# Kernel optimization log

Measured on AMD Instinct MI355X. Metric: run time of the kernel, lower is better.

Reference implementation:

```python
import math
import jax, jax.numpy as jnp
import numpy as np

HEADS = 2
HEAD_NUMS = 4
BS, C, NR, NC = 16, 256, 96, 96


def _sa(x, mask, kw, kb, qw, qb, vw, vb):
    # x: [B, C, N] (Conv1d k=1 == per-position linear), mask: [B, N] floats in {0,1}
    B, Cc, N = x.shape
    H = HEAD_NUMS
    D = Cc // H
    scale = 1.0 / math.sqrt(D)

    def proj(w, b):
        return (jnp.einsum('dc,bcn->bdn', w, x) + b[None, :, None]).reshape(B, H, D, N)

    k = proj(kw, kb)
    q = proj(qw, qb)
    v = proj(vw, vb)
    # logits[b,h,n,m] = sum_d k[b,h,d,n] * q[b,h,d,m]; softmax over m, mask on m
    logits = jnp.einsum('bhdn,bhdm->bhnm', k, q) * scale
    mbool = mask > 0
    logits = jnp.where(mbool[:, None, None, :], logits, jnp.asarray(-1e30, x.dtype))
    w = jax.nn.softmax(logits, axis=-1)
    out = jnp.einsum('bhdm,bhnm->bhdn', v, w).reshape(B, Cc, N)
    # fully-masked sequences (padded grid rows/cols) -> zero instead of NaN
    valid = jnp.any(mbool, axis=-1)  # [B]
    out = jnp.where(valid[:, None, None], out, jnp.zeros((), x.dtype))
    return out + x


def setup_inputs() -> dict:
    key = jax.random.key(0)
    ks = jax.random.split(key, 16)
    num_rows = jax.random.randint(ks[0], (BS,), NR // 2, NR + 1, dtype=jnp.int32)
    num_cols = jax.random.randint(ks[1], (BS,), NC // 2, NC + 1, dtype=jnp.int32)
    feats = jax.random.normal(ks[2], (BS, C, NR, NC), dtype=jnp.float32)
    # aligned cell features are zero in padded region (align_cells_feat pads with 0)
    rmask = (jnp.arange(NR)[None, :] < num_rows[:, None])
    cmask = (jnp.arange(NC)[None, :] < num_cols[:, None])
    grid = (rmask[:, :, None] & cmask[:, None, :]).astype(jnp.float32)
    feats = feats * grid[:, None, :, :]
    inp = {'feats': feats, 'num_rows': num_rows, 'num_cols': num_cols}
    names = ['col_k', 'col_q', 'col_v', 'row_k', 'row_q', 'row_v']
    for i, nm in enumerate(names):
        inp[nm + '_w'] = 0.02 * jax.random.normal(ks[3 + 2 * i], (HEADS, C, C), dtype=jnp.float32)
        inp[nm + '_b'] = 0.02 * jax.random.normal(ks[4 + 2 * i], (HEADS, C), dtype=jnp.float32)
    return inp


def reference(feats, num_rows, num_cols,
              col_k_w, col_k_b, col_q_w, col_q_b, col_v_w, col_v_b,
              row_k_w, row_k_b, row_q_w, row_q_b, row_v_w, row_v_b):
    bs, c, nr, nc = feats.shape
    rmask = (jnp.arange(nr)[None, :] < num_rows[:, None])
    cmask = (jnp.arange(nc)[None, :] < num_cols[:, None])
    masks = (rmask[:, :, None] & cmask[:, None, :]).astype(feats.dtype)  # [bs, nr, nc]
    x = feats
    for i in range(HEADS):
        # column attention: sequences along nc, one per (batch, row)
        xc = x.transpose(0, 2, 1, 3).reshape(bs * nr, c, nc)
        mc = masks.reshape(bs * nr, nc)
        xc = _sa(xc, mc, col_k_w[i], col_k_b[i], col_q_w[i], col_q_b[i], col_v_w[i], col_v_b[i])
        x = xc.reshape(bs, nr, c, nc).transpose(0, 2, 1, 3)
        # row attention: sequences along nr, one per (batch, col)
        xr = x.transpose(0, 3, 1, 2).reshape(bs * nc, c, nr)
        mr = masks.transpose(0, 2, 1).reshape(bs * nc, nr)
        xr = _sa(xr, mr, row_k_w[i], row_k_b[i], row_q_w[i], row_q_b[i], row_v_w[i], row_v_b[i])
        x = xr.reshape(bs, nc, c, nr).transpose(0, 2, 3, 1)
    return x, masks
```

## Files before the change

### kernel.cpp

```cpp
#include <hip/hip_runtime.h>

typedef __attribute__((ext_vector_type(8))) short bf16x8;
typedef __attribute__((ext_vector_type(4))) float f32x4;

#define MFMA16(a, b, c) __builtin_amdgcn_mfma_f32_16x16x32_bf16(a, b, c, 0, 0, 0)

__device__ __forceinline__ unsigned short f2bf(float f) {
    unsigned int u = __float_as_uint(f);
    u += 0x7FFFu + ((u >> 16) & 1u);
    return (unsigned short)(u >> 16);
}
__device__ __forceinline__ float bf2f(unsigned short h) {
    return __uint_as_float(((unsigned int)h) << 16);
}

struct WPtrs { const float* p[6]; };

__global__ __launch_bounds__(256) void conv_w_kernel(WPtrs wp, unsigned short* dst) {
    int idx = blockIdx.x * 256 + threadIdx.x;
    if (idx >= 196608) return;
    int t = idx >> 15;
    int q = idx & 32767;
    float4 v = *(const float4*)(wp.p[t] + ((size_t)q << 2));
    ushort4 o;
    o.x = f2bf(v.x); o.y = f2bf(v.y); o.z = f2bf(v.z); o.w = f2bf(v.w);
    *(ushort4*)(dst + ((size_t)t << 17) + ((size_t)q << 2)) = o;
}

__global__ __launch_bounds__(256) void conv_in_kernel(const float* __restrict__ src,
                                                      unsigned short* __restrict__ dst, int n4) {
    for (int i = blockIdx.x * 256 + threadIdx.x; i < n4; i += gridDim.x * 256) {
        float4 v = *(const float4*)(src + 4 * (size_t)i);
        ushort4 o;
        o.x = f2bf(v.x); o.y = f2bf(v.y); o.z = f2bf(v.z); o.w = f2bf(v.w);
        *(ushort4*)(dst + 4 * (size_t)i) = o;
    }
}

__global__ __launch_bounds__(256) void transpose_ip(unsigned short* __restrict__ x) {
    __shared__ unsigned short t[96 * 98];
    const size_t base = (size_t)blockIdx.x * 9216;
    for (int i = threadIdx.x; i < 2304; i += 256) {
        int r = i / 24, c4 = (i % 24) * 4;
        ushort4 v = *(const ushort4*)(x + base + r * 96 + c4);
        t[r * 98 + c4 + 0] = v.x; t[r * 98 + c4 + 1] = v.y;
        t[r * 98 + c4 + 2] = v.z; t[r * 98 + c4 + 3] = v.w;
    }
    __syncthreads();
    for (int i = threadIdx.x; i < 2304; i += 256) {
        int r = i / 24, c4 = (i % 24) * 4;
        ushort4 o;
        o.x = t[(c4 + 0) * 98 + r]; o.y = t[(c4 + 1) * 98 + r];
        o.z = t[(c4 + 2) * 98 + r]; o.w = t[(c4 + 3) * 98 + r];
        *(ushort4*)(x + base + r * 96 + c4) = o;
    }
}

__global__ __launch_bounds__(256) void final_t(const unsigned short* __restrict__ x,
                                               float* __restrict__ out) {
    __shared__ unsigned short t[96 * 98];
    const size_t base = (size_t)blockIdx.x * 9216;
    for (int i = threadIdx.x; i < 2304; i += 256) {
        int r = i / 24, c4 = (i % 24) * 4;
        ushort4 v = *(const ushort4*)(x + base + r * 96 + c4);
        t[r * 98 + c4 + 0] = v.x; t[r * 98 + c4 + 1] = v.y;
        t[r * 98 + c4 + 2] = v.z; t[r * 98 + c4 + 3] = v.w;
    }
    __syncthreads();
    for (int i = threadIdx.x; i < 2304; i += 256) {
        int r = i / 24, c4 = (i % 24) * 4;
        float4 f;
        f.x = bf2f(t[(c4 + 0) * 98 + r]); f.y = bf2f(t[(c4 + 1) * 98 + r]);
        f.z = bf2f(t[(c4 + 2) * 98 + r]); f.w = bf2f(t[(c4 + 3) * 98 + r]);
        *(float4*)(out + base + r * 96 + c4) = f;
    }
}

__global__ __launch_bounds__(256) void masks_kernel(const int* __restrict__ nr,
                                                    const int* __restrict__ nc,
                                                    float* __restrict__ out) {
    int i = blockIdx.x * 256 + threadIdx.x;
    if (i >= 147456) return;
    int b = i / 9216, rem = i % 9216, r = rem / 96, c = rem % 96;
    out[i] = (r < nr[b] && c < nc[b]) ? 1.0f : 0.0f;
}

#define XT_S 40
#define KT_S 72
#define VM_S 104
#define PM_S 104
#define OT_S 100

__global__ __launch_bounds__(384, 3) void sa2(
    const unsigned short* __restrict__ src, unsigned short* __restrict__ dst,
    const unsigned short* __restrict__ Wk, const unsigned short* __restrict__ Wq,
    const unsigned short* __restrict__ Wv,
    const float* __restrict__ bk, const float* __restrict__ bq, const float* __restrict__ bv,
    const int* __restrict__ lim_s, const int* __restrict__ lim_m) {
    extern __shared__ char smem[];
    unsigned short* xt = (unsigned short*)smem;
    unsigned short* Kt = (unsigned short*)(smem + 7680);
    unsigned short* Qt = (unsigned short*)(smem + 21504);
    unsigned short* Vm = (unsigned short*)(smem + 35328);
    unsigned short* Pm = (unsigned short*)(smem + 48640);
    float*          OT = (float*)smem;

    const int bid = blockIdx.x;
    const int h   = bid & 3;
    const int seq = bid >> 2;
    const int b = seq / 96, s = seq % 96;
    const int tid = threadIdx.x;

    const size_t slab = (size_t)b * 2359296 + (size_t)s * 96;
    const unsigned short* sg = src + slab;
    unsigned short* dg = dst + slab;

    if (s >= lim_s[b]) {
        for (int i = tid; i < 768; i += 384) {
            int c = h * 64 + i / 12, o8 = (i % 12) * 8;
            *(uint4*)(dg + (size_t)c * 9216 + o8) = *(const uint4*)(sg + (size_t)c * 9216 + o8);
        }
        return;
    }
    const int mlim = lim_m[b];

    const int wave = tid >> 6, lane = tid & 63, lr = lane & 15, lk = lane >> 4;
    const int p = wave >> 1, g = wave & 1;
    const unsigned short* Wp = (p == 0) ? Wk : (p == 1) ? Wq : Wv;
    const float* bp = (p == 0) ? bk : (p == 1) ? bq : bv;

    const int cloc = tid / 12, oc = tid % 12;
    f32x4 acc[2][6];
#pragma unroll
    for (int dt = 0; dt < 2; ++dt)
#pragma unroll
        for (int nt = 0; nt < 6; ++nt) acc[dt][nt] = (f32x4)0.0f;

    uint4 v = *(const uint4*)(sg + (size_t)cloc * 9216 + oc * 8);
#pragma unroll
    for (int cc = 0; cc < 8; ++cc) {
        __syncthreads();
        {
            const unsigned short* pv = (const unsigned short*)&v;
#pragma unroll
            for (int j = 0; j < 8; ++j) {
                const int jj = (j + cloc) & 7;
                xt[(oc * 8 + jj) * XT_S + cloc] = pv[jj];
            }
        }
        __syncthreads();
        if (cc < 7) v = *(const uint4*)(sg + (size_t)((cc + 1) * 32 + cloc) * 9216 + oc * 8);
        bf16x8 bfr[6];
#pragma unroll
        for (int nt = 0; nt < 6; ++nt)
            bfr[nt] = *(const bf16x8*)&xt[(nt * 16 + lr) * XT_S + lk * 8];
#pragma unroll
        for (int dt = 0; dt < 2; ++dt) {
            bf16x8 afr = *(const bf16x8*)&Wp[(size_t)(h * 64 + g * 32 + dt * 16 + lr) * 256 + cc * 32 + lk * 8];
#pragma unroll
            for (int nt = 0; nt < 6; ++nt)
                acc[dt][nt] = MFMA16(afr, bfr[nt], acc[dt][nt]);
        }
    }

#pragma unroll
    for (int dt = 0; dt < 2; ++dt) {
        const int dbase = g * 32 + dt * 16 + lk * 4;
        const float b0 = bp[h * 64 + dbase + 0], b1 = bp[h * 64 + dbase + 1];
        const float b2 = bp[h * 64 + dbase + 2], b3 = bp[h * 64 + dbase + 3];
#pragma unroll
        for (int nt = 0; nt < 6; ++nt) {
            const int n = nt * 16 + lr;
            if (p == 2) {
                Vm[(dbase + 0) * VM_S + n] = f2bf(acc[dt][nt][0] + b0);
                Vm[(dbase + 1) * VM_S + n] = f2bf(acc[dt][nt][1] + b1);
                Vm[(dbase + 2) * VM_S + n] = f2bf(acc[dt][nt][2] + b2);
                Vm[(dbase + 3) * VM_S + n] = f2bf(acc[dt][nt][3] + b3);
            } else {
                ushort4 o;
                o.x = f2bf(acc[dt][nt][0] + b0);
                o.y = f2bf(acc[dt][nt][1] + b1);
                o.z = f2bf(acc[dt][nt][2] + b2);
                o.w = f2bf(acc[dt][nt][3] + b3);
                *(ushort4*)&((p == 0 ? Kt : Qt)[n * KT_S + dbase]) = o;
            }
        }
    }
    __syncthreads();

    f32x4 acc2[6];
#pragma unroll
    for (int mt = 0; mt < 6; ++mt) acc2[mt] = (f32x4)0.0f;
#pragma unroll
    for (int k0 = 0; k0 < 64; k0 += 32) {
        bf16x8 kf = *(const bf16x8*)&Kt[(wave * 16 + lr) * KT_S + k0 + lk * 8];
#pragma unroll
        for (int mt = 0; mt < 6; ++mt) {
            bf16x8 qf = *(const bf16x8*)&Qt[(mt * 16 + lr) * KT_S + k0 + lk * 8];
            acc2[mt] = MFMA16(kf, qf, acc2[mt]);
        }
    }

    float lg[6][4];
#pragma unroll
    for (int mt = 0; mt < 6; ++mt) {
        const bool valid = (mt * 16 + lr) < mlim;
#pragma unroll
        for (int r2 = 0; r2 < 4; ++r2)
            lg[mt][r2] = valid ? acc2[mt][r2] * 0.125f : -3.0e38f;
    }
#pragma unroll
    for (int r2 = 0; r2 < 4; ++r2) {
        float mx = lg[0][r2];
#pragma unroll
        for (int mt = 1; mt < 6; ++mt) mx = fmaxf(mx, lg[mt][r2]);
        mx = fmaxf(mx, __shfl_xor(mx, 1));
        mx = fmaxf(mx, __shfl_xor(mx, 2));
        mx = fmaxf(mx, __shfl_xor(mx, 4));
        mx = fmaxf(mx, __shfl_xor(mx, 8));
        float sm = 0.0f;
#pragma unroll
        for (int mt = 0; mt < 6; ++mt) {
            float e = __expf(lg[mt][r2] - mx);
            lg[mt][r2] = e;
            sm += e;
        }
        sm += __shfl_xor(sm, 1);
        sm += __shfl_xor(sm, 2);
        sm += __shfl_xor(sm, 4);
        sm += __shfl_xor(sm, 8);
        const float inv = 1.0f / sm;
        const int n = wave * 16 + lk * 4 + r2;
#pragma unroll
        for (int mt = 0; mt < 6; ++mt)
            Pm[n * PM_S + mt * 16 + lr] = f2bf(lg[mt][r2] * inv);
    }
    __syncthreads();

    f32x4 acc3[4];
#pragma unroll
    for (int dt = 0; dt < 4; ++dt) acc3[dt] = (f32x4)0.0f;
    const int nk = (mlim + 31) >> 5;
    for (int k0i = 0; k0i < nk; ++k0i) {
        const int k0 = k0i * 32;
        bf16x8 pf = *(const bf16x8*)&Pm[(wave * 16 + lr) * PM_S + k0 + lk * 8];
#pragma unroll
        for (int dt = 0; dt < 4; ++dt) {
            bf16x8 vf = *(const bf16x8*)&Vm[(dt * 16 + lr) * VM_S + k0 + lk * 8];
            acc3[dt] = MFMA16(vf, pf, acc3[dt]);
        }
    }

#pragma unroll
    for (int dt = 0; dt < 4; ++dt)
#pragma unroll
        for (int r2 = 0; r2 < 4; ++r2)
            OT[(dt * 16 + lk * 4 + r2) * OT_S + wave * 16 + lr] = acc3[dt][r2];
    __syncthreads();
    for (int i = tid; i < 768; i += 384) {
        const int c = i / 12, o8 = (i % 12) * 8;
        const size_t ga = (size_t)(h * 64 + c) * 9216 + o8;
        uint4 rv = *(const uint4*)(sg + ga);
        const unsigned short* rs = (const unsigned short*)&rv;
        unsigned short ob[8];
#pragma unroll
        for (int j = 0; j < 8; ++j)
            ob[j] = f2bf(OT[c * OT_S + o8 + j] + bf2f(rs[j]));
        *(uint4*)(dg + ga) = *(const uint4*)ob;
    }
}

extern "C" void kernel_launch(void* const* d_in, const int* in_sizes, int n_in,
                              void* d_out, int out_size, void* d_ws, size_t ws_size,
                              hipStream_t stream) {
    const float* feats    = (const float*)d_in[0];
    const int*   num_rows = (const int*)d_in[1];
    const int*   num_cols = (const int*)d_in[2];

    unsigned short* bufA = (unsigned short*)d_ws;
    unsigned short* wbuf = (unsigned short*)((char*)d_ws + 75497472);
    unsigned short* bufB = (unsigned short*)d_out;

    WPtrs wp;
    for (int t = 0; t < 6; ++t) wp.p[t] = (const float*)d_in[3 + 2 * t];

    (void)hipFuncSetAttribute((const void*)sa2,
                              hipFuncAttributeMaxDynamicSharedMemorySize, 68608);

    conv_w_kernel<<<768, 256, 0, stream>>>(wp, wbuf);
    conv_in_kernel<<<2048, 256, 0, stream>>>(feats, bufA, 9437184);

    unsigned short* cur = bufA;
    unsigned short* nxt = bufB;
    for (int i = 0; i < 2; ++i) {
        for (int dir = 0; dir < 2; ++dir) {
            const int tb = dir * 3;
            const unsigned short* Wk = wbuf + (size_t)(tb + 0) * 131072 + (size_t)i * 65536;
            const unsigned short* Wq = wbuf + (size_t)(tb + 1) * 131072 + (size_t)i * 65536;
            const unsigned short* Wv = wbuf + (size_t)(tb + 2) * 131072 + (size_t)i * 65536;
            const float* bk = (const float*)d_in[4 + 2 * (tb + 0)] + i * 256;
            const float* bq = (const float*)d_in[4 + 2 * (tb + 1)] + i * 256;
            const float* bv = (const float*)d_in[4 + 2 * (tb + 2)] + i * 256;
            const int* lim_s = (dir == 0) ? num_rows : num_cols;
            const int* lim_m = (dir == 0) ? num_cols : num_rows;
            sa2<<<6144, 384, 68608, stream>>>(cur, nxt, Wk, Wq, Wv, bk, bq, bv, lim_s, lim_m);
            unsigned short* t = cur; cur = nxt; nxt = t;
            if (!(i == 1 && dir == 1))
                transpose_ip<<<4096, 256, 0, stream>>>(cur);
        }
    }

    final_t<<<4096, 256, 0, stream>>>(cur, (float*)d_out);
    masks_kernel<<<576, 256, 0, stream>>>(num_rows, num_cols, (float*)d_out + 37748736);
}
```

Baseline: 1.328 ms.

## Switch to channel-last layout with transposing writes, dropping separate transpose passes

The activation layout becomes channel-innermost ([b, r, c, C]). The attention kernel now reads B fragments straight from global memory without the LDS staging transpose, and writes its output already transposed for the next direction, so the three transpose_ip launches go away. The input conversion and final output kernels now also transpose. Shared memory is reused across phases (Pm/OT alias Kt), which cuts it to 40KB and lifts occupancy to 4 blocks, at the cost of extra barriers. Blocks are also reordered so neighbouring sequences share weight and cache locality.

```diff
diff --git a/kernel.cpp b/kernel.cpp
--- a/kernel.cpp
+++ b/kernel.cpp
@@ -27,52 +27,51 @@
     *(ushort4*)(dst + ((size_t)t << 17) + ((size_t)q << 2)) = o;
 }
 
-__global__ __launch_bounds__(256) void conv_in_kernel(const float* __restrict__ src,
-                                                      unsigned short* __restrict__ dst, int n4) {
-    for (int i = blockIdx.x * 256 + threadIdx.x; i < n4; i += gridDim.x * 256) {
-        float4 v = *(const float4*)(src + 4 * (size_t)i);
-        ushort4 o;
-        o.x = f2bf(v.x); o.y = f2bf(v.y); o.z = f2bf(v.z); o.w = f2bf(v.w);
-        *(ushort4*)(dst + 4 * (size_t)i) = o;
-    }
-}
-
-__global__ __launch_bounds__(256) void transpose_ip(unsigned short* __restrict__ x) {
-    __shared__ unsigned short t[96 * 98];
-    const size_t base = (size_t)blockIdx.x * 9216;
-    for (int i = threadIdx.x; i < 2304; i += 256) {
-        int r = i / 24, c4 = (i % 24) * 4;
-        ushort4 v = *(const ushort4*)(x + base + r * 96 + c4);
-        t[r * 98 + c4 + 0] = v.x; t[r * 98 + c4 + 1] = v.y;
-        t[r * 98 + c4 + 2] = v.z; t[r * 98 + c4 + 3] = v.w;
-    }
-    __syncthreads();
-    for (int i = threadIdx.x; i < 2304; i += 256) {
-        int r = i / 24, c4 = (i % 24) * 4;
-        ushort4 o;
-        o.x = t[(c4 + 0) * 98 + r]; o.y = t[(c4 + 1) * 98 + r];
-        o.z = t[(c4 + 2) * 98 + r]; o.w = t[(c4 + 3) * 98 + r];
-        *(ushort4*)(x + base + r * 96 + c4) = o;
-    }
-}
-
-__global__ __launch_bounds__(256) void final_t(const unsigned short* __restrict__ x,
+__global__ __launch_bounds__(256) void t_in(const float* __restrict__ feats,
+                                            unsigned short* __restrict__ dst) {
+    __shared__ unsigned short t[96 * 257];
+    const int b = blockIdx.x / 96, r = blockIdx.x % 96;
+    const int tid = threadIdx.x;
+    for (int i = tid; i < 6144; i += 256) {
+        const int c = i / 24, q4 = i % 24;
+        float4 v = *(const float4*)(feats + ((size_t)(b * 256 + c) * 9216) + r * 96 + q4 * 4);
+        t[(q4 * 4 + 0) * 257 + c] = f2bf(v.x);
+        t[(q4 * 4 + 1) * 257 + c] = f2bf(v.y);
+        t[(q4 * 4 + 2) * 257 + c] = f2bf(v.z);
+        t[(q4 * 4 + 3) * 257 + c] = f2bf(v.w);
+    }
+    __syncthreads();
+    for (int i = tid; i < 3072; i += 256) {
+        const int q = i / 32, co = i % 32;
+        unsigned short ob[8];
+#pragma unroll
+        for (int j = 0; j < 8; ++j) ob[j] = t[q * 257 + co * 8 + j];
+        *(uint4*)(dst + ((size_t)(b * 96 + r) * 96 + q) * 256 + co * 8) = *(const uint4*)ob;
+    }
+}
+
+__global__ __launch_bounds__(256) void final_k(const unsigned short* __restrict__ x,
                                                float* __restrict__ out) {
-    __shared__ unsigned short t[96 * 98];
-    const size_t base = (size_t)blockIdx.x * 9216;
-    for (int i = threadIdx.x; i < 2304; i += 256) {
-        int r = i / 24, c4 = (i % 24) * 4;
-        ushort4 v = *(const ushort4*)(x + base + r * 96 + c4);
-        t[r * 98 + c4 + 0] = v.x; t[r * 98 + c4 + 1] = v.y;
-        t[r * 98 + c4 + 2] = v.z; t[r * 98 + c4 + 3] = v.w;
-    }
-    __syncthreads();
-    for (int i = threadIdx.x; i < 2304; i += 256) {
-        int r = i / 24, c4 = (i % 24) * 4;
+    __shared__ unsigned short t[256 * 97];
+    const int b = blockIdx.x / 96, r = blockIdx.x % 96;
+    const int tid = threadIdx.x;
+    const unsigned short* sg = x + (size_t)(b * 96 + r) * 24576;
+    for (int i = tid; i < 3072; i += 256) {
+        const int q = i / 32, co = i % 32;
+        uint4 v = *(const uint4*)(sg + (size_t)q * 256 + co * 8);
+        const unsigned short* pv = (const unsigned short*)&v;
+#pragma unroll
+        for (int j = 0; j < 8; ++j) t[(co * 8 + j) * 97 + q] = pv[j];
+    }
+    __syncthreads();
+    for (int i = tid; i < 6144; i += 256) {
+        const int c = i / 24, q4 = i % 24;
         float4 f;
-        f.x = bf2f(t[(c4 + 0) * 98 + r]); f.y = bf2f(t[(c4 + 1) * 98 + r]);
-        f.z = bf2f(t[(c4 + 2) * 98 + r]); f.w = bf2f(t[(c4 + 3) * 98 + r]);
-        *(float4*)(out + base + r * 96 + c4) = f;
+        f.x = bf2f(t[c * 97 + q4 * 4 + 0]);
+        f.y = bf2f(t[c * 97 + q4 * 4 + 1]);
+        f.z = bf2f(t[c * 97 + q4 * 4 + 2]);
+        f.w = bf2f(t[c * 97 + q4 * 4 + 3]);
+        *(float4*)(out + ((size_t)(b * 256 + c) * 9216) + r * 96 + q4 * 4) = f;
     }
 }
 
@@ -85,40 +84,38 @@
     out[i] = (r < nr[b] && c < nc[b]) ? 1.0f : 0.0f;
 }
 
-#define XT_S 40
 #define KT_S 72
 #define VM_S 104
 #define PM_S 104
-#define OT_S 100
-
-__global__ __launch_bounds__(384, 3) void sa2(
+#define OT_S 101
+
+__global__ __launch_bounds__(384, 4) void sa3(
     const unsigned short* __restrict__ src, unsigned short* __restrict__ dst,
     const unsigned short* __restrict__ Wk, const unsigned short* __restrict__ Wq,
     const unsigned short* __restrict__ Wv,
     const float* __restrict__ bk, const float* __restrict__ bq, const float* __restrict__ bv,
     const int* __restrict__ lim_s, const int* __restrict__ lim_m) {
     extern __shared__ char smem[];
-    unsigned short* xt = (unsigned short*)smem;
-    unsigned short* Kt = (unsigned short*)(smem + 7680);
-    unsigned short* Qt = (unsigned short*)(smem + 21504);
-    unsigned short* Vm = (unsigned short*)(smem + 35328);
-    unsigned short* Pm = (unsigned short*)(smem + 48640);
+    unsigned short* Kt = (unsigned short*)smem;
+    unsigned short* Qt = (unsigned short*)(smem + 13824);
+    unsigned short* Vm = (unsigned short*)(smem + 27648);
+    unsigned short* Pm = (unsigned short*)smem;
     float*          OT = (float*)smem;
 
     const int bid = blockIdx.x;
-    const int h   = bid & 3;
-    const int seq = bid >> 2;
+    const int grp = bid >> 5, l5 = bid & 31;
+    const int h = l5 >> 3;
+    const int seq = grp * 8 + (l5 & 7);
     const int b = seq / 96, s = seq % 96;
     const int tid = threadIdx.x;
 
-    const size_t slab = (size_t)b * 2359296 + (size_t)s * 96;
-    const unsigned short* sg = src + slab;
-    unsigned short* dg = dst + slab;
+    const unsigned short* sg = src + (size_t)seq * 24576;
 
     if (s >= lim_s[b]) {
         for (int i = tid; i < 768; i += 384) {
-            int c = h * 64 + i / 12, o8 = (i % 12) * 8;
-            *(uint4*)(dg + (size_t)c * 9216 + o8) = *(const uint4*)(sg + (size_t)c * 9216 + o8);
+            const int n = i >> 3, c8 = i & 7;
+            uint4 v = *(const uint4*)(sg + (size_t)n * 256 + h * 64 + c8 * 8);
+            *(uint4*)(dst + ((size_t)(b * 96 + n) * 96 + s) * 256 + h * 64 + c8 * 8) = v;
         }
         return;
     }
@@ -129,39 +126,30 @@
     const unsigned short* Wp = (p == 0) ? Wk : (p == 1) ? Wq : Wv;
     const float* bp = (p == 0) ? bk : (p == 1) ? bq : bv;
 
-    const int cloc = tid / 12, oc = tid % 12;
     f32x4 acc[2][6];
 #pragma unroll
     for (int dt = 0; dt < 2; ++dt)
 #pragma unroll
         for (int nt = 0; nt < 6; ++nt) acc[dt][nt] = (f32x4)0.0f;
 
-    uint4 v = *(const uint4*)(sg + (size_t)cloc * 9216 + oc * 8);
+    const unsigned short* xb = sg + lr * 256 + lk * 8;
+    const unsigned short* wb = Wp + (size_t)(h * 64 + g * 32 + lr) * 256 + lk * 8;
 #pragma unroll
     for (int cc = 0; cc < 8; ++cc) {
-        __syncthreads();
-        {
-            const unsigned short* pv = (const unsigned short*)&v;
-#pragma unroll
-            for (int j = 0; j < 8; ++j) {
-                const int jj = (j + cloc) & 7;
-                xt[(oc * 8 + jj) * XT_S + cloc] = pv[jj];
-            }
-        }
-        __syncthreads();
-        if (cc < 7) v = *(const uint4*)(sg + (size_t)((cc + 1) * 32 + cloc) * 9216 + oc * 8);
         bf16x8 bfr[6];
 #pragma unroll
         for (int nt = 0; nt < 6; ++nt)
-            bfr[nt] = *(const bf16x8*)&xt[(nt * 16 + lr) * XT_S + lk * 8];
+            bfr[nt] = *(const bf16x8*)(xb + nt * 4096 + cc * 32);
 #pragma unroll
         for (int dt = 0; dt < 2; ++dt) {
-            bf16x8 afr = *(const bf16x8*)&Wp[(size_t)(h * 64 + g * 32 + dt * 16 + lr) * 256 + cc * 32 + lk * 8];
+            bf16x8 afr = *(const bf16x8*)(wb + dt * 4096 + cc * 32);
 #pragma unroll
             for (int nt = 0; nt < 6; ++nt)
                 acc[dt][nt] = MFMA16(afr, bfr[nt], acc[dt][nt]);
         }
     }
+
+    __syncthreads();
 
 #pragma unroll
     for (int dt = 0; dt < 2; ++dt) {
@@ -200,6 +188,7 @@
             acc2[mt] = MFMA16(kf, qf, acc2[mt]);
         }
     }
+    __syncthreads();
 
     float lg[6][4];
 #pragma unroll
@@ -250,6 +239,7 @@
             acc3[dt] = MFMA16(vf, pf, acc3[dt]);
         }
     }
+    __syncthreads();
 
 #pragma unroll
     for (int dt = 0; dt < 4; ++dt)
@@ -257,16 +247,16 @@
         for (int r2 = 0; r2 < 4; ++r2)
             OT[(dt * 16 + lk * 4 + r2) * OT_S + wave * 16 + lr] = acc3[dt][r2];
     __syncthreads();
+
     for (int i = tid; i < 768; i += 384) {
-        const int c = i / 12, o8 = (i % 12) * 8;
-        const size_t ga = (size_t)(h * 64 + c) * 9216 + o8;
-        uint4 rv = *(const uint4*)(sg + ga);
+        const int n = i >> 3, c8 = i & 7;
+        uint4 rv = *(const uint4*)(sg + (size_t)n * 256 + h * 64 + c8 * 8);
         const unsigned short* rs = (const unsigned short*)&rv;
         unsigned short ob[8];
 #pragma unroll
         for (int j = 0; j < 8; ++j)
-            ob[j] = f2bf(OT[c * OT_S + o8 + j] + bf2f(rs[j]));
-        *(uint4*)(dg + ga) = *(const uint4*)ob;
+            ob[j] = f2bf(OT[(c8 * 8 + j) * OT_S + n] + bf2f(rs[j]));
+        *(uint4*)(dst + ((size_t)(b * 96 + n) * 96 + s) * 256 + h * 64 + c8 * 8) = *(const uint4*)ob;
     }
 }
 
@@ -284,11 +274,11 @@
     WPtrs wp;
     for (int t = 0; t < 6; ++t) wp.p[t] = (const float*)d_in[3 + 2 * t];
 
-    (void)hipFuncSetAttribute((const void*)sa2,
-                              hipFuncAttributeMaxDynamicSharedMemorySize, 68608);
+    (void)hipFuncSetAttribute((const void*)sa3,
+                              hipFuncAttributeMaxDynamicSharedMemorySize, 40960);
 
     conv_w_kernel<<<768, 256, 0, stream>>>(wp, wbuf);
-    conv_in_kernel<<<2048, 256, 0, stream>>>(feats, bufA, 9437184);
+    t_in<<<1536, 256, 0, stream>>>(feats, bufA);
 
     unsigned short* cur = bufA;
     unsigned short* nxt = bufB;
@@ -303,13 +293,11 @@
             const float* bv = (const float*)d_in[4 + 2 * (tb + 2)] + i * 256;
             const int* lim_s = (dir == 0) ? num_rows : num_cols;
             const int* lim_m = (dir == 0) ? num_cols : num_rows;
-            sa2<<<6144, 384, 68608, stream>>>(cur, nxt, Wk, Wq, Wv, bk, bq, bv, lim_s, lim_m);
+            sa3<<<6144, 384, 40960, stream>>>(cur, nxt, Wk, Wq, Wv, bk, bq, bv, lim_s, lim_m);
             unsigned short* t = cur; cur = nxt; nxt = t;
-            if (!(i == 1 && dir == 1))
-                transpose_ip<<<4096, 256, 0, stream>>>(cur);
-        }
-    }
-
-    final_t<<<4096, 256, 0, stream>>>(cur, (float*)d_out);
+        }
+    }
+
+    final_k<<<1536, 256, 0, stream>>>(cur, (float*)d_out);
     masks_kernel<<<576, 256, 0, stream>>>(num_rows, num_cols, (float*)d_out + 37748736);
 }
```

Result: slower. 1.386 ms (+4.4%).
